# Kernel tuning notes

Hardware: AMD Instinct MI355X
Metric: run time of the kernel (lower is better)

Reference implementation:

```python
import jax, jax.numpy as jnp
import numpy as np

INPUT_DIM = 512
HIDDEN_DIM = 512


def _linear_params(key, in_dim, out_dim):
    kw, kb = jax.random.split(key)
    bound = 1.0 / np.sqrt(in_dim)
    W = jax.random.uniform(kw, (out_dim, in_dim), minval=-bound, maxval=bound, dtype=jnp.float32)
    b = jax.random.uniform(kb, (out_dim,), minval=-bound, maxval=bound, dtype=jnp.float32)
    return W, b


def setup_inputs() -> dict:
    key = jax.random.key(0)
    keys = jax.random.split(key, 11)
    B = 8192
    inp = {
        "x_t": jax.random.normal(keys[0], (B, INPUT_DIM), dtype=jnp.float32),
        "h_tm1": jax.random.normal(keys[1], (B, HIDDEN_DIM), dtype=jnp.float32),
        "c_tm1": jax.random.normal(keys[2], (B, HIDDEN_DIM), dtype=jnp.float32),
    }
    names = ["f_x", "f_h", "i_x", "i_h", "g_x", "g_h", "o_x", "o_h"]
    for n, k in zip(names, keys[3:]):
        in_dim = INPUT_DIM if n.endswith("_x") else HIDDEN_DIM
        W, b = _linear_params(k, in_dim, HIDDEN_DIM)
        inp[f"W_{n}"] = W
        inp[f"b_{n}"] = b
    return inp


def reference(x_t, h_tm1, c_tm1,
              W_f_x, b_f_x, W_f_h, b_f_h,
              W_i_x, b_i_x, W_i_h, b_i_h,
              W_g_x, b_g_x, W_g_h, b_g_h,
              W_o_x, b_o_x, W_o_h, b_o_h):
    # Stacked weights: [4, H, D] -> einsum over D gives [B, 4, H].
    Wx = jnp.stack([W_f_x, W_g_x, W_i_x, W_o_x])  # [4, H, Din]
    bx = jnp.stack([b_f_x, b_g_x, b_i_x, b_o_x])  # [4, H]
    Wh = jnp.stack([W_f_h, W_g_h, W_i_h, W_o_h])
    bh = jnp.stack([b_f_h, b_g_h, b_i_h, b_o_h])
    pre = (jnp.einsum('bd,ghd->bgh', x_t, Wx) + bx
           + jnp.einsum('bd,ghd->bgh', h_tm1, Wh) + bh)  # [B, 4, H]
    f_t = jax.nn.sigmoid(pre[:, 0])
    g_t = jnp.tanh(pre[:, 1])
    i_t = jax.nn.sigmoid(pre[:, 2])
    o_t = jax.nn.sigmoid(pre[:, 3])
    c_t = f_t * c_tm1 + i_t * g_t
    h_t = o_t * jnp.tanh(c_t)
    return (h_t, c_t)
```

## Files before the change

### kernel.cpp

```cpp
#include <hip/hip_runtime.h>
#include <cstdint>
#include <cstddef>


typedef __attribute__((ext_vector_type(8))) short short8;
typedef __attribute__((ext_vector_type(4))) float floatx4;

#define AS1(p) ((const __attribute__((address_space(1))) void*)(p))
#define AS3(p) ((__attribute__((address_space(3))) void*)(p))

__device__ __forceinline__ unsigned short f2bf(float f) {
  union { float f; unsigned u; } v; v.f = f;
  unsigned u = v.u;
  return (unsigned short)((u + 0x7fffu + ((u >> 16) & 1u)) >> 16);
}

struct PackArgs {
  const float* x; const float* h;
  const float* wx[4]; const float* wh[4];
  const float* bx[4]; const float* bh[4];
  unsigned short* A; unsigned short* B; float* bias;
};

__global__ __launch_bounds__(256) void pack_all_kernel(PackArgs P) {
  const int bid = blockIdx.x;
  if (bid < 8192) {
    int e = (bid * 256 + threadIdx.x) * 4;
    int b = e >> 10, k = e & 1023;
    const float* src = (k < 512) ? (P.x + b * 512 + k)
                                 : (P.h + b * 512 + (k - 512));
    float4 v = *(const float4*)src;
    ushort4 o;
    o.x = f2bf(v.x); o.y = f2bf(v.y); o.z = f2bf(v.z); o.w = f2bf(v.w);
    *(ushort4*)(P.A + e) = o;
  } else {
    int e = ((bid - 8192) * 256 + threadIdx.x) * 4;
    int n = e >> 10, k = e & 1023;
    int g = n >> 9, hh = n & 511;
    const float* src = (k < 512) ? (P.wx[g] + hh * 512 + k)
                                 : (P.wh[g] + hh * 512 + (k - 512));
    float4 v = *(const float4*)src;
    ushort4 o;
    o.x = f2bf(v.x); o.y = f2bf(v.y); o.z = f2bf(v.z); o.w = f2bf(v.w);
    *(ushort4*)(P.B + e) = o;
    if (k == 0) P.bias[n] = P.bx[g][hh] + P.bh[g][hh];
  }
}

__global__ __launch_bounds__(512, 4)
void lstm_gemm_kernel(const unsigned short* __restrict__ A,
                      const unsigned short* __restrict__ B,
                      const float* __restrict__ bias,
                      const float* __restrict__ c_prev,
                      float* __restrict__ h_out,
                      float* __restrict__ c_out) {
  __shared__ __align__(16) char smem[49152];
  __shared__ float biasS[128];

  const int tid  = threadIdx.x;
  const int lane = tid & 63;
  const int w    = tid >> 6;
  const int quad = lane >> 4;
  const int colA = lane & 15;
  const int m0   = blockIdx.x * 256;
  const int h0   = blockIdx.y * 32;

  if (tid < 128) {
    biasS[tid] = bias[(tid >> 5) * 512 + h0 + (tid & 31)];
  }

  const int srow = tid >> 3;
  const int cl   = tid & 7;
  const int cg   = cl ^ (srow & 7);

  floatx4 acc[4][4];
#pragma unroll
  for (int i = 0; i < 4; ++i)
#pragma unroll
    for (int j = 0; j < 4; ++j) acc[i][j] = (floatx4){0.f, 0.f, 0.f, 0.f};

  const int wm = (w >> 1) * 64;
  const int wn = (w & 1) * 64;

  const char* Ag = (const char*)A;
  const char* Bg = (const char*)B;

  for (int kt = 0; kt < 16; ++kt) {
    __syncthreads();
    const int kb = kt * 128;
#pragma unroll
    for (int j = 0; j < 4; ++j) {
      int r = j * 64 + srow;
      __builtin_amdgcn_global_load_lds(
          AS1(Ag + (size_t)(m0 + r) * 2048 + kb + cg * 16),
          AS3(smem + r * 128 + cl * 16), 16, 0, 0);
    }
#pragma unroll
    for (int j = 0; j < 2; ++j) {
      int r = j * 64 + srow;
      int grow = (r >> 5) * 512 + h0 + (r & 31);
      __builtin_amdgcn_global_load_lds(
          AS1(Bg + (size_t)grow * 2048 + kb + cg * 16),
          AS3(smem + 32768 + r * 128 + cl * 16), 16, 0, 0);
    }
    __syncthreads();

#pragma unroll
    for (int kk = 0; kk < 2; ++kk) {
      const int off = ((kk * 4 + quad) ^ (colA & 7)) * 16;
      short8 af[4], bfr[4];
#pragma unroll
      for (int mi = 0; mi < 4; ++mi)
        af[mi] = *(const short8*)(smem + (wm + mi * 16 + colA) * 128 + off);
#pragma unroll
      for (int ni = 0; ni < 4; ++ni)
        bfr[ni] = *(const short8*)(smem + 32768 + (wn + ni * 16 + colA) * 128 + off);
#pragma unroll
      for (int mi = 0; mi < 4; ++mi)
#pragma unroll
        for (int ni = 0; ni < 4; ++ni)
          acc[mi][ni] = __builtin_amdgcn_mfma_f32_16x16x32_bf16(
              af[mi], bfr[ni], acc[mi][ni], 0, 0, 0);
    }
  }

  __syncthreads();
  float* ep = (float*)smem;
#pragma unroll
  for (int rd = 0; rd < 4; ++rd) {
    if ((w >> 1) == rd) {
#pragma unroll
      for (int mi = 0; mi < 4; ++mi)
#pragma unroll
        for (int ni = 0; ni < 4; ++ni) {
          int rr0 = mi * 16 + quad * 4;
          int cc  = wn + ni * 16 + colA;
#pragma unroll
          for (int rr = 0; rr < 4; ++rr)
            ep[(rr0 + rr) * 132 + cc] = acc[mi][ni][rr];
        }
    }
    __syncthreads();
#pragma unroll
    for (int j = 0; j < 4; ++j) {
      int idx  = j * 512 + tid;
      int mloc = idx >> 5;
      int hh   = idx & 31;
      float pf = ep[mloc * 132 +      hh] + biasS[hh];
      float pi = ep[mloc * 132 + 32 + hh] + biasS[32 + hh];
      float pg = ep[mloc * 132 + 64 + hh] + biasS[64 + hh];
      float po = ep[mloc * 132 + 96 + hh] + biasS[96 + hh];
      float fg = 1.f / (1.f + __expf(-pf));
      float ig = 1.f / (1.f + __expf(-pi));
      float gg = 1.f - 2.f / (1.f + __expf(2.f * pg));
      float og = 1.f / (1.f + __expf(-po));
      int m  = m0 + rd * 64 + mloc;
      int hg = h0 + hh;
      float cp = c_prev[m * 512 + hg];
      float cv = fg * cp + ig * gg;
      float th = 1.f - 2.f / (1.f + __expf(2.f * cv));
      h_out[m * 512 + hg] = og * th;
      c_out[m * 512 + hg] = cv;
    }
    __syncthreads();
  }
}

extern "C" void kernel_launch(void* const* d_in, const int* in_sizes, int n_in,
                              void* d_out, int out_size, void* d_ws, size_t ws_size,
                              hipStream_t stream) {
  char* ws = (char*)d_ws;
  unsigned short* Abf = (unsigned short*)ws;
  unsigned short* Bbf = (unsigned short*)(ws + (size_t)16777216);
  float* bias = (float*)(ws + (size_t)16777216 + 4194304);

  float* hout = (float*)d_out;
  float* cout = hout + (size_t)8192 * 512;

  PackArgs P;
  P.x = (const float*)d_in[0];
  P.h = (const float*)d_in[1];
  P.wx[0] = (const float*)d_in[3];  P.bx[0] = (const float*)d_in[4];
  P.wh[0] = (const float*)d_in[5];  P.bh[0] = (const float*)d_in[6];
  P.wx[1] = (const float*)d_in[7];  P.bx[1] = (const float*)d_in[8];
  P.wh[1] = (const float*)d_in[9];  P.bh[1] = (const float*)d_in[10];
  P.wx[2] = (const float*)d_in[11]; P.bx[2] = (const float*)d_in[12];
  P.wh[2] = (const float*)d_in[13]; P.bh[2] = (const float*)d_in[14];
  P.wx[3] = (const float*)d_in[15]; P.bx[3] = (const float*)d_in[16];
  P.wh[3] = (const float*)d_in[17]; P.bh[3] = (const float*)d_in[18];
  P.A = Abf; P.B = Bbf; P.bias = bias;

  pack_all_kernel<<<10240, 256, 0, stream>>>(P);

  const float* c = (const float*)d_in[2];
  dim3 grid(32, 16);
  lstm_gemm_kernel<<<grid, 512, 0, stream>>>(Abf, Bbf, bias, c, hout, cout);
}
```

Measured before the change: 167.6 us.

## Warp-specialize GEMM into producer waves and MFMA waves with triple-buffered LDS

Splits the block into 4 loader waves that stream A/B tiles into a 3-stage LDS ring via global_load_lds and 8 compute waves that run MFMAs. Stages are coordinated with shared-memory atomic counters and spin-waits instead of block-wide barriers. The goal is to overlap global loads with MFMA work inside one block. In exchange the kernel uses about 144KB of LDS, limiting occupancy to one block per CU, and it relies on spin-polling synchronisation.

```diff
diff --git a/kernel.cpp b/kernel.cpp
--- a/kernel.cpp
+++ b/kernel.cpp
@@ -47,80 +47,102 @@
   }
 }
 
-__global__ __launch_bounds__(512, 4)
+__global__ __launch_bounds__(768)
 void lstm_gemm_kernel(const unsigned short* __restrict__ A,
                       const unsigned short* __restrict__ B,
                       const float* __restrict__ bias,
                       const float* __restrict__ c_prev,
                       float* __restrict__ h_out,
                       float* __restrict__ c_out) {
-  __shared__ __align__(16) char smem[49152];
+  __shared__ __align__(16) char smem[147456];
   __shared__ float biasS[128];
+  __shared__ int prod_cnt[3];
+  __shared__ int cons_cnt[3];
 
   const int tid  = threadIdx.x;
   const int lane = tid & 63;
   const int w    = tid >> 6;
+  const int m0   = blockIdx.x * 256;
+  const int h0   = blockIdx.y * 32;
+
+  if (tid < 3) { prod_cnt[tid] = 0; cons_cnt[tid] = 0; }
+  if (tid < 128) biasS[tid] = bias[(tid >> 5) * 512 + h0 + (tid & 31)];
+  __syncthreads();
+
   const int quad = lane >> 4;
   const int colA = lane & 15;
-  const int m0   = blockIdx.x * 256;
-  const int h0   = blockIdx.y * 32;
-
-  if (tid < 128) {
-    biasS[tid] = bias[(tid >> 5) * 512 + h0 + (tid & 31)];
-  }
-
-  const int srow = tid >> 3;
-  const int cl   = tid & 7;
-  const int cg   = cl ^ (srow & 7);
-
-  floatx4 acc[4][4];
-#pragma unroll
-  for (int i = 0; i < 4; ++i)
-#pragma unroll
-    for (int j = 0; j < 4; ++j) acc[i][j] = (floatx4){0.f, 0.f, 0.f, 0.f};
-
   const int wm = (w >> 1) * 64;
   const int wn = (w & 1) * 64;
 
-  const char* Ag = (const char*)A;
-  const char* Bg = (const char*)B;
-
-  for (int kt = 0; kt < 16; ++kt) {
-    __syncthreads();
-    const int kb = kt * 128;
-#pragma unroll
-    for (int j = 0; j < 4; ++j) {
-      int r = j * 64 + srow;
-      __builtin_amdgcn_global_load_lds(
-          AS1(Ag + (size_t)(m0 + r) * 2048 + kb + cg * 16),
-          AS3(smem + r * 128 + cl * 16), 16, 0, 0);
-    }
-#pragma unroll
-    for (int j = 0; j < 2; ++j) {
-      int r = j * 64 + srow;
-      int grow = (r >> 5) * 512 + h0 + (r & 31);
-      __builtin_amdgcn_global_load_lds(
-          AS1(Bg + (size_t)grow * 2048 + kb + cg * 16),
-          AS3(smem + 32768 + r * 128 + cl * 16), 16, 0, 0);
-    }
-    __syncthreads();
-
-#pragma unroll
-    for (int kk = 0; kk < 2; ++kk) {
-      const int off = ((kk * 4 + quad) ^ (colA & 7)) * 16;
-      short8 af[4], bfr[4];
-#pragma unroll
-      for (int mi = 0; mi < 4; ++mi)
-        af[mi] = *(const short8*)(smem + (wm + mi * 16 + colA) * 128 + off);
-#pragma unroll
-      for (int ni = 0; ni < 4; ++ni)
-        bfr[ni] = *(const short8*)(smem + 32768 + (wn + ni * 16 + colA) * 128 + off);
-#pragma unroll
-      for (int mi = 0; mi < 4; ++mi)
+  floatx4 acc[4][4];
+#pragma unroll
+  for (int i = 0; i < 4; ++i)
+#pragma unroll
+    for (int j = 0; j < 4; ++j) acc[i][j] = (floatx4){0.f, 0.f, 0.f, 0.f};
+
+  if (w >= 8) {
+    const int p  = w - 8;
+    const char* Ag = (const char*)A;
+    const char* Bg = (const char*)B;
+    const int lrow = lane >> 3;
+    const int cl   = lane & 7;
+    const int cg   = cl ^ lrow;
+    for (int kt = 0; kt < 16; ++kt) {
+      const int s = kt % 3;
+      const int g = kt / 3;
+      if (g > 0) {
+        while (__atomic_load_n(&cons_cnt[s], __ATOMIC_ACQUIRE) < 8 * g)
+          __builtin_amdgcn_s_sleep(1);
+      }
+      const int kb = kt * 128;
+      char* sb = smem + s * 49152;
+#pragma unroll
+      for (int i = 0; i < 12; ++i) {
+        const int t = p + 4 * i;
+        if (t < 32) {
+          int r = t * 8 + lrow;
+          __builtin_amdgcn_global_load_lds(
+              AS1(Ag + (size_t)(m0 + r) * 2048 + kb + cg * 16),
+              AS3(sb + r * 128 + cl * 16), 16, 0, 0);
+        } else {
+          int r = (t - 32) * 8 + lrow;
+          int grow = (r >> 5) * 512 + h0 + (r & 31);
+          __builtin_amdgcn_global_load_lds(
+              AS1(Bg + (size_t)grow * 2048 + kb + cg * 16),
+              AS3(sb + 32768 + r * 128 + cl * 16), 16, 0, 0);
+        }
+      }
+      __builtin_amdgcn_s_waitcnt(0x0F70);
+      if (lane == 0)
+        __atomic_fetch_add(&prod_cnt[s], 1, __ATOMIC_RELEASE);
+    }
+  } else {
+    for (int kt = 0; kt < 16; ++kt) {
+      const int s = kt % 3;
+      const int g = kt / 3;
+      while (__atomic_load_n(&prod_cnt[s], __ATOMIC_ACQUIRE) < 4 * (g + 1))
+        __builtin_amdgcn_s_sleep(1);
+      const char* Ab = smem + s * 49152;
+      const char* Bb = Ab + 32768;
+#pragma unroll
+      for (int kk = 0; kk < 2; ++kk) {
+        const int off = ((kk * 4 + quad) ^ (colA & 7)) * 16;
+        short8 af[4], bfr[4];
+#pragma unroll
+        for (int mi = 0; mi < 4; ++mi)
+          af[mi] = *(const short8*)(Ab + (wm + mi * 16 + colA) * 128 + off);
 #pragma unroll
         for (int ni = 0; ni < 4; ++ni)
-          acc[mi][ni] = __builtin_amdgcn_mfma_f32_16x16x32_bf16(
-              af[mi], bfr[ni], acc[mi][ni], 0, 0, 0);
+          bfr[ni] = *(const short8*)(Bb + (wn + ni * 16 + colA) * 128 + off);
+#pragma unroll
+        for (int mi = 0; mi < 4; ++mi)
+#pragma unroll
+          for (int ni = 0; ni < 4; ++ni)
+            acc[mi][ni] = __builtin_amdgcn_mfma_f32_16x16x32_bf16(
+                af[mi], bfr[ni], acc[mi][ni], 0, 0, 0);
+      }
+      if (lane == 0)
+        __atomic_fetch_add(&cons_cnt[s], 1, __ATOMIC_RELEASE);
     }
   }
 
@@ -128,7 +150,7 @@
   float* ep = (float*)smem;
 #pragma unroll
   for (int rd = 0; rd < 4; ++rd) {
-    if ((w >> 1) == rd) {
+    if (w < 8 && (w >> 1) == rd) {
 #pragma unroll
       for (int mi = 0; mi < 4; ++mi)
 #pragma unroll
@@ -142,25 +164,27 @@
     }
     __syncthreads();
 #pragma unroll
-    for (int j = 0; j < 4; ++j) {
-      int idx  = j * 512 + tid;
-      int mloc = idx >> 5;
-      int hh   = idx & 31;
-      float pf = ep[mloc * 132 +      hh] + biasS[hh];
-      float pi = ep[mloc * 132 + 32 + hh] + biasS[32 + hh];
-      float pg = ep[mloc * 132 + 64 + hh] + biasS[64 + hh];
-      float po = ep[mloc * 132 + 96 + hh] + biasS[96 + hh];
-      float fg = 1.f / (1.f + __expf(-pf));
-      float ig = 1.f / (1.f + __expf(-pi));
-      float gg = 1.f - 2.f / (1.f + __expf(2.f * pg));
-      float og = 1.f / (1.f + __expf(-po));
-      int m  = m0 + rd * 64 + mloc;
-      int hg = h0 + hh;
-      float cp = c_prev[m * 512 + hg];
-      float cv = fg * cp + ig * gg;
-      float th = 1.f - 2.f / (1.f + __expf(2.f * cv));
-      h_out[m * 512 + hg] = og * th;
-      c_out[m * 512 + hg] = cv;
+    for (int j = 0; j < 3; ++j) {
+      int idx = j * 768 + tid;
+      if (idx < 2048) {
+        int mloc = idx >> 5;
+        int hh   = idx & 31;
+        float pf = ep[mloc * 132 +      hh] + biasS[hh];
+        float pi = ep[mloc * 132 + 32 + hh] + biasS[32 + hh];
+        float pg = ep[mloc * 132 + 64 + hh] + biasS[64 + hh];
+        float po = ep[mloc * 132 + 96 + hh] + biasS[96 + hh];
+        float fg = 1.f / (1.f + __expf(-pf));
+        float ig = 1.f / (1.f + __expf(-pi));
+        float gg = 1.f - 2.f / (1.f + __expf(2.f * pg));
+        float og = 1.f / (1.f + __expf(-po));
+        int m  = m0 + rd * 64 + mloc;
+        int hg = h0 + hh;
+        float cp = c_prev[m * 512 + hg];
+        float cv = fg * cp + ig * gg;
+        float th = 1.f - 2.f / (1.f + __expf(2.f * cv));
+        h_out[m * 512 + hg] = og * th;
+        c_out[m * 512 + hg] = cv;
+      }
     }
     __syncthreads();
   }
@@ -194,5 +218,5 @@
 
   const float* c = (const float*)d_in[2];
   dim3 grid(32, 16);
-  lstm_gemm_kernel<<<grid, 512, 0, stream>>>(Abf, Bbf, bias, c, hout, cout);
-}
+  lstm_gemm_kernel<<<grid, 768, 0, stream>>>(Abf, Bbf, bias, c, hout, cout);
+}
```

After: 178.9 us. 6.8% more time.
